# Optimization experiments

Hardware: AMD Instinct MI355X
Metric: run time of the kernel (lower is better)

## Reference

```python
import jax, jax.numpy as jnp
import numpy as np

N, E = 50000, 800000
IN, HID, HEADS = 512, 64, 2
NEG_SLOPE = 0.2

def _p(key, shape, fan_in):
    return jax.random.normal(key, shape, dtype=jnp.float32) * (1.0 / np.sqrt(fan_in))

def setup_inputs() -> dict:
    key = jax.random.key(0)
    ks = jax.random.split(key, 16)
    x = jax.random.normal(ks[0], (N, IN), dtype=jnp.float32)
    edge_index = jax.random.randint(ks[1], (2, E), 0, N)
    d = dict(x=x, edge_index=edge_index)
    # layer 0: in -> hidden*heads
    d['W0'] = _p(ks[2], (IN, HEADS * HID), IN)
    d['a_src0'] = _p(ks[3], (HEADS, HID), HID)
    d['a_dst0'] = _p(ks[4], (HEADS, HID), HID)
    d['b0'] = jnp.zeros((HEADS * HID,), jnp.float32)
    # layer 1: hidden*heads -> hidden*heads
    d['W1'] = _p(ks[5], (HEADS * HID, HEADS * HID), HEADS * HID)
    d['a_src1'] = _p(ks[6], (HEADS, HID), HID)
    d['a_dst1'] = _p(ks[7], (HEADS, HID), HID)
    d['b1'] = jnp.zeros((HEADS * HID,), jnp.float32)
    # layer 2: hidden*heads -> hidden, heads=1
    d['W2'] = _p(ks[8], (HEADS * HID, HID), HEADS * HID)
    d['a_src2'] = _p(ks[9], (1, HID), HID)
    d['a_dst2'] = _p(ks[10], (1, HID), HID)
    d['b2'] = jnp.zeros((HID,), jnp.float32)
    # MLP heads
    d['Wv'] = _p(ks[11], (HID, HID), HID)
    d['bv'] = jnp.zeros((HID,), jnp.float32)
    d['Wt'] = _p(ks[12], (HID, HID), HID)
    d['bt'] = jnp.zeros((HID,), jnp.float32)
    return d

def gat_conv(x, src, dst, W, a_src, a_dst, b, n_nodes):
    # PyG GATConv: linear -> per-node att scores -> edge leaky_relu -> segment softmax over dst -> weighted scatter-sum
    H, C = a_src.shape
    h = (x @ W).reshape(n_nodes, H, C)                     # [N,H,C]
    s = jnp.einsum('nhc,hc->nh', h, a_src)                 # [N,H]
    t = jnp.einsum('nhc,hc->nh', h, a_dst)                 # [N,H]
    e = jax.nn.leaky_relu(s[src] + t[dst], NEG_SLOPE)      # [Etot,H]
    m = jax.ops.segment_max(e, dst, num_segments=n_nodes)  # stable softmax per dst
    ex = jnp.exp(e - m[dst])
    den = jax.ops.segment_sum(ex, dst, num_segments=n_nodes)
    alpha = ex / (den[dst] + 1e-16)                        # [Etot,H]
    out = jax.ops.segment_sum(h[src] * alpha[..., None], dst, num_segments=n_nodes)
    return out.reshape(n_nodes, H * C) + b

def reference(x, edge_index, W0, a_src0, a_dst0, b0, W1, a_src1, a_dst1, b1,
              W2, a_src2, a_dst2, b2, Wv, bv, Wt, bt):
    n = x.shape[0]
    loop = jnp.arange(n)
    src = jnp.concatenate([edge_index[0], loop])  # add_self_loops=True
    dst = jnp.concatenate([edge_index[1], loop])
    h = gat_conv(x, src, dst, W0, a_src0, a_dst0, b0, n)
    h = jax.nn.relu(h)
    h = gat_conv(h, src, dst, W1, a_src1, a_dst1, b1, n)
    h = jax.nn.relu(h)
    h = gat_conv(h, src, dst, W2, a_src2, a_dst2, b2, n)  # heads=1 -> [N,HID]
    x_vision = jax.nn.relu(h @ Wv + bv)
    x_text = jax.nn.relu(h @ Wt + bt)
    return (h, x_vision, x_text)
```

## Files before the change

### kernel.cpp

```cpp
#include <hip/hip_runtime.h>
#include <hip/hip_bf16.h>
#include <hip/hip_fp16.h>
#include <math.h>

#define NN 50000
#define NE 800000

typedef unsigned short ushort_t;
typedef unsigned int uint_t;
typedef __attribute__((ext_vector_type(8))) short bf16x8;
typedef __attribute__((ext_vector_type(4))) float f32x4;

__device__ __forceinline__ float lrelu(float x) { return x >= 0.f ? x : 0.2f * x; }

__device__ __forceinline__ ushort_t f2bf_rn(float f) {
  uint_t u = __builtin_bit_cast(uint_t, f);
  uint_t r = u + 0x7FFFu + ((u >> 16) & 1u);
  return (ushort_t)(r >> 16);
}
__device__ __forceinline__ float bf2f(ushort_t h) {
  uint_t u = ((uint_t)h) << 16;
  return __builtin_bit_cast(float, u);
}

__global__ void count_kernel(const int* __restrict__ ei, int* __restrict__ counts, int E) {
  int e = blockIdx.x * blockDim.x + threadIdx.x;
  if (e < E) atomicAdd(&counts[ei[E + e]], 1);
}

__global__ __launch_bounds__(256) void scan_blocksum_kernel(const int* __restrict__ counts,
                                                            int* __restrict__ bsums, int n) {
  __shared__ int red[4];
  int i = blockIdx.x * 256 + threadIdx.x;
  int v = (i < n) ? counts[i] : 0;
#pragma unroll
  for (int off = 32; off > 0; off >>= 1) v += __shfl_down(v, off);
  if ((threadIdx.x & 63) == 0) red[threadIdx.x >> 6] = v;
  __syncthreads();
  if (threadIdx.x == 0) bsums[blockIdx.x] = red[0] + red[1] + red[2] + red[3];
}

__global__ __launch_bounds__(256) void scan_offsets_kernel(int* __restrict__ bsums, int nb) {
  __shared__ int sm[256];
  int tid = threadIdx.x;
  int v = (tid < nb) ? bsums[tid] : 0;
  sm[tid] = v;
  __syncthreads();
  for (int off = 1; off < 256; off <<= 1) {
    int u = (tid >= off) ? sm[tid - off] : 0;
    __syncthreads();
    sm[tid] += u;
    __syncthreads();
  }
  if (tid < nb) bsums[tid] = sm[tid] - v;
}

__global__ __launch_bounds__(256) void scan_final_kernel(const int* __restrict__ counts,
                                                         const int* __restrict__ boffs,
                                                         int* __restrict__ row_ptr, int n, int E) {
  __shared__ int sm[256];
  int tid = threadIdx.x;
  int i = blockIdx.x * 256 + tid;
  int v = (i < n) ? counts[i] : 0;
  int orig = v;
  sm[tid] = v;
  __syncthreads();
  for (int off = 1; off < 256; off <<= 1) {
    int u = (tid >= off) ? sm[tid - off] : 0;
    __syncthreads();
    sm[tid] += u;
    __syncthreads();
  }
  if (i < n) row_ptr[i] = boffs[blockIdx.x] + sm[tid] - orig;
  if (i == n) row_ptr[n] = E;
}

__global__ void fill_kernel(const int* __restrict__ ei, const int* __restrict__ row_ptr,
                            int* __restrict__ cursor, int* __restrict__ col_src, int E) {
  int e = blockIdx.x * blockDim.x + threadIdx.x;
  if (e < E) {
    int d = ei[E + e];
    int pos = row_ptr[d] + atomicAdd(&cursor[d], 1);
    col_src[pos] = ei[e];
  }
}

__global__ void prep_wt_kernel(const float* __restrict__ W, int Kdim, int C,
                               ushort_t* __restrict__ wth, ushort_t* __restrict__ wtl) {
  int t = blockIdx.x * blockDim.x + threadIdx.x;
  int nk = Kdim >> 4;
  if (t >= C * nk) return;
  int c = t / nk, kc = (t % nk) << 4;
  uint_t hw[8], lw[8];
#pragma unroll
  for (int i = 0; i < 8; ++i) {
    float f0 = W[(size_t)(kc + 2 * i) * C + c];
    float f1 = W[(size_t)(kc + 2 * i + 1) * C + c];
    ushort_t h0 = f2bf_rn(f0), h1 = f2bf_rn(f1);
    ushort_t l0 = f2bf_rn(f0 - bf2f(h0)), l1 = f2bf_rn(f1 - bf2f(h1));
    hw[i] = (uint_t)h0 | ((uint_t)h1 << 16);
    lw[i] = (uint_t)l0 | ((uint_t)l1 << 16);
  }
  uint_t* ph = (uint_t*)&wth[(size_t)c * Kdim + kc];
  uint_t* pl = (uint_t*)&wtl[(size_t)c * Kdim + kc];
  *(uint4*)ph = make_uint4(hw[0], hw[1], hw[2], hw[3]);
  *(uint4*)(ph + 4) = make_uint4(hw[4], hw[5], hw[6], hw[7]);
  *(uint4*)pl = make_uint4(lw[0], lw[1], lw[2], lw[3]);
  *(uint4*)(pl + 4) = make_uint4(lw[4], lw[5], lw[6], lw[7]);
}

template <int K>
__global__ __launch_bounds__(256, 2) void gemm_mfma_kernel(const float* __restrict__ A,
                                                           const ushort_t* __restrict__ wth,
                                                           const ushort_t* __restrict__ wtl,
                                                           float* __restrict__ out, int n) {
  __shared__ __align__(16) ushort_t ah[128][40];
  __shared__ __align__(16) ushort_t al[128][40];
  __shared__ __align__(16) ushort_t bh[128][40];
  __shared__ __align__(16) ushort_t bl[128][40];

  const int t = threadIdx.x;
  const int row0 = blockIdx.x * 128;
  const int srow = t >> 1;
  const int skq = (t & 1) * 16;

  const int lane = t & 63;
  const int wid = t >> 6;
  const int wm = wid >> 1, wn = wid & 1;
  const int r16 = lane & 15, g = lane >> 4;

  f32x4 acc[4][4];
#pragma unroll
  for (int i = 0; i < 4; ++i)
#pragma unroll
    for (int j = 0; j < 4; ++j) acc[i][j] = (f32x4)(0.f);

  for (int kt = 0; kt < K / 32; ++kt) {
    const int k0 = kt * 32;
    {
      uint_t hw[8], lw[8];
      if (row0 + srow < n) {
        const float* ap = &A[(size_t)(row0 + srow) * K + k0 + skq];
#pragma unroll
        for (int j = 0; j < 4; ++j) {
          float4 v = *(const float4*)(ap + j * 4);
          ushort_t h0 = f2bf_rn(v.x), h1 = f2bf_rn(v.y), h2 = f2bf_rn(v.z), h3 = f2bf_rn(v.w);
          ushort_t l0 = f2bf_rn(v.x - bf2f(h0)), l1 = f2bf_rn(v.y - bf2f(h1));
          ushort_t l2 = f2bf_rn(v.z - bf2f(h2)), l3 = f2bf_rn(v.w - bf2f(h3));
          hw[j * 2] = (uint_t)h0 | ((uint_t)h1 << 16);
          hw[j * 2 + 1] = (uint_t)h2 | ((uint_t)h3 << 16);
          lw[j * 2] = (uint_t)l0 | ((uint_t)l1 << 16);
          lw[j * 2 + 1] = (uint_t)l2 | ((uint_t)l3 << 16);
        }
      } else {
#pragma unroll
        for (int j = 0; j < 8; ++j) { hw[j] = 0; lw[j] = 0; }
      }
      *(uint4*)&ah[srow][skq] = make_uint4(hw[0], hw[1], hw[2], hw[3]);
      *(uint4*)&ah[srow][skq + 8] = make_uint4(hw[4], hw[5], hw[6], hw[7]);
      *(uint4*)&al[srow][skq] = make_uint4(lw[0], lw[1], lw[2], lw[3]);
      *(uint4*)&al[srow][skq + 8] = make_uint4(lw[4], lw[5], lw[6], lw[7]);
    }
    {
      const ushort_t* ph = &wth[(size_t)srow * K + k0 + skq];
      const ushort_t* pl = &wtl[(size_t)srow * K + k0 + skq];
      uint4 vh0 = *(const uint4*)ph;
      uint4 vh1 = *(const uint4*)(ph + 8);
      uint4 vl0 = *(const uint4*)pl;
      uint4 vl1 = *(const uint4*)(pl + 8);
      *(uint4*)&bh[srow][skq] = vh0;
      *(uint4*)&bh[srow][skq + 8] = vh1;
      *(uint4*)&bl[srow][skq] = vl0;
      *(uint4*)&bl[srow][skq + 8] = vl1;
    }
    __syncthreads();

    bf16x8 fah[4], fal[4], fbh[4], fbl[4];
#pragma unroll
    for (int mf = 0; mf < 4; ++mf) {
      fah[mf] = *(const bf16x8*)&ah[wm * 64 + mf * 16 + r16][g * 8];
      fal[mf] = *(const bf16x8*)&al[wm * 64 + mf * 16 + r16][g * 8];
    }
#pragma unroll
    for (int nf = 0; nf < 4; ++nf) {
      fbh[nf] = *(const bf16x8*)&bh[wn * 64 + nf * 16 + r16][g * 8];
      fbl[nf] = *(const bf16x8*)&bl[wn * 64 + nf * 16 + r16][g * 8];
    }
#pragma unroll
    for (int mf = 0; mf < 4; ++mf)
#pragma unroll
      for (int nf = 0; nf < 4; ++nf) {
        acc[mf][nf] = __builtin_amdgcn_mfma_f32_16x16x32_bf16(fah[mf], fbh[nf], acc[mf][nf], 0, 0, 0);
        acc[mf][nf] = __builtin_amdgcn_mfma_f32_16x16x32_bf16(fah[mf], fbl[nf], acc[mf][nf], 0, 0, 0);
        acc[mf][nf] = __builtin_amdgcn_mfma_f32_16x16x32_bf16(fal[mf], fbh[nf], acc[mf][nf], 0, 0, 0);
      }
    __syncthreads();
  }

#pragma unroll
  for (int mf = 0; mf < 4; ++mf) {
#pragma unroll
    for (int reg = 0; reg < 4; ++reg) {
      int row = row0 + wm * 64 + mf * 16 + g * 4 + reg;
      if (row < n) {
#pragma unroll
        for (int nf = 0; nf < 4; ++nf) {
          out[(size_t)row * 128 + wn * 64 + nf * 16 + r16] = acc[mf][nf][reg];
        }
      }
    }
  }
}

template <int K>
__global__ __launch_bounds__(256, 2) void gemm_mfma64_kernel(const float* __restrict__ A,
                                                             const ushort_t* __restrict__ wth,
                                                             const ushort_t* __restrict__ wtl,
                                                             const float* __restrict__ bias,
                                                             int do_relu,
                                                             float* __restrict__ out, int n) {
  __shared__ __align__(16) ushort_t ah[128][40];
  __shared__ __align__(16) ushort_t al[128][40];
  __shared__ __align__(16) ushort_t bh[64][40];
  __shared__ __align__(16) ushort_t bl[64][40];

  const int t = threadIdx.x;
  const int row0 = blockIdx.x * 128;
  const int srow = t >> 1;
  const int skq = (t & 1) * 16;
  const int bcol = t >> 2;
  const int bkq = (t & 3) * 8;

  const int lane = t & 63;
  const int wid = t >> 6;
  const int r16 = lane & 15, g = lane >> 4;

  f32x4 acc[2][4];
#pragma unroll
  for (int i = 0; i < 2; ++i)
#pragma unroll
    for (int j = 0; j < 4; ++j) acc[i][j] = (f32x4)(0.f);

  for (int kt = 0; kt < K / 32; ++kt) {
    const int k0 = kt * 32;
    {
      uint_t hw[8], lw[8];
      if (row0 + srow < n) {
        const float* ap = &A[(size_t)(row0 + srow) * K + k0 + skq];
#pragma unroll
        for (int j = 0; j < 4; ++j) {
          float4 v = *(const float4*)(ap + j * 4);
          ushort_t h0 = f2bf_rn(v.x), h1 = f2bf_rn(v.y), h2 = f2bf_rn(v.z), h3 = f2bf_rn(v.w);
          ushort_t l0 = f2bf_rn(v.x - bf2f(h0)), l1 = f2bf_rn(v.y - bf2f(h1));
          ushort_t l2 = f2bf_rn(v.z - bf2f(h2)), l3 = f2bf_rn(v.w - bf2f(h3));
          hw[j * 2] = (uint_t)h0 | ((uint_t)h1 << 16);
          hw[j * 2 + 1] = (uint_t)h2 | ((uint_t)h3 << 16);
          lw[j * 2] = (uint_t)l0 | ((uint_t)l1 << 16);
          lw[j * 2 + 1] = (uint_t)l2 | ((uint_t)l3 << 16);
        }
      } else {
#pragma unroll
        for (int j = 0; j < 8; ++j) { hw[j] = 0; lw[j] = 0; }
      }
      *(uint4*)&ah[srow][skq] = make_uint4(hw[0], hw[1], hw[2], hw[3]);
      *(uint4*)&ah[srow][skq + 8] = make_uint4(hw[4], hw[5], hw[6], hw[7]);
      *(uint4*)&al[srow][skq] = make_uint4(lw[0], lw[1], lw[2], lw[3]);
      *(uint4*)&al[srow][skq + 8] = make_uint4(lw[4], lw[5], lw[6], lw[7]);
    }
    {
      uint4 vh = *(const uint4*)&wth[(size_t)bcol * K + k0 + bkq];
      uint4 vl = *(const uint4*)&wtl[(size_t)bcol * K + k0 + bkq];
      *(uint4*)&bh[bcol][bkq] = vh;
      *(uint4*)&bl[bcol][bkq] = vl;
    }
    __syncthreads();

    bf16x8 fah[2], fal[2], fbh[4], fbl[4];
#pragma unroll
    for (int mf = 0; mf < 2; ++mf) {
      fah[mf] = *(const bf16x8*)&ah[wid * 32 + mf * 16 + r16][g * 8];
      fal[mf] = *(const bf16x8*)&al[wid * 32 + mf * 16 + r16][g * 8];
    }
#pragma unroll
    for (int nf = 0; nf < 4; ++nf) {
      fbh[nf] = *(const bf16x8*)&bh[nf * 16 + r16][g * 8];
      fbl[nf] = *(const bf16x8*)&bl[nf * 16 + r16][g * 8];
    }
#pragma unroll
    for (int mf = 0; mf < 2; ++mf)
#pragma unroll
      for (int nf = 0; nf < 4; ++nf) {
        acc[mf][nf] = __builtin_amdgcn_mfma_f32_16x16x32_bf16(fah[mf], fbh[nf], acc[mf][nf], 0, 0, 0);
        acc[mf][nf] = __builtin_amdgcn_mfma_f32_16x16x32_bf16(fah[mf], fbl[nf], acc[mf][nf], 0, 0, 0);
        acc[mf][nf] = __builtin_amdgcn_mfma_f32_16x16x32_bf16(fal[mf], fbh[nf], acc[mf][nf], 0, 0, 0);
      }
    __syncthreads();
  }

#pragma unroll
  for (int mf = 0; mf < 2; ++mf) {
#pragma unroll
    for (int reg = 0; reg < 4; ++reg) {
      int row = row0 + wid * 32 + mf * 16 + g * 4 + reg;
      if (row < n) {
#pragma unroll
        for (int nf = 0; nf < 4; ++nf) {
          int col = nf * 16 + r16;
          float v = acc[mf][nf][reg];
          if (bias) v += bias[col];
          if (do_relu) v = fmaxf(v, 0.f);
          out[(size_t)row * 64 + col] = v;
        }
      }
    }
  }
}

__global__ __launch_bounds__(256) void comb_att2_kernel(const float* __restrict__ P0,
                                                        const float* __restrict__ a_src,
                                                        const float* __restrict__ a_dst,
                                                        __half2* __restrict__ h2h,
                                                        float2* __restrict__ s2,
                                                        float2* __restrict__ t2, int n) {
  int wid = (blockIdx.x * 256 + threadIdx.x) >> 6;
  int lane = threadIdx.x & 63;
  if (wid >= n) return;
  float h0 = P0[(size_t)wid * 128 + lane];
  float h1 = P0[(size_t)wid * 128 + 64 + lane];
  h2h[(size_t)wid * 64 + lane] = __floats2half2_rn(h0, h1);
  float v0 = h0 * a_src[lane];
  float v1 = h1 * a_src[64 + lane];
  float v2 = h0 * a_dst[lane];
  float v3 = h1 * a_dst[64 + lane];
#pragma unroll
  for (int off = 32; off > 0; off >>= 1) {
    v0 += __shfl_xor(v0, off);
    v1 += __shfl_xor(v1, off);
    v2 += __shfl_xor(v2, off);
    v3 += __shfl_xor(v3, off);
  }
  if (lane == 0) {
    s2[wid] = make_float2(v0, v1);
    t2[wid] = make_float2(v2, v3);
  }
}

__global__ __launch_bounds__(256) void att1_kernel(const float* __restrict__ h,
                                                   const float* __restrict__ a_src,
                                                   const float* __restrict__ a_dst,
                                                   float* __restrict__ s, float* __restrict__ t,
                                                   __half* __restrict__ h16, int n) {
  int wid = (blockIdx.x * 256 + threadIdx.x) >> 6;
  int lane = threadIdx.x & 63;
  if (wid >= n) return;
  float h0 = h[(size_t)wid * 64 + lane];
  h16[(size_t)wid * 64 + lane] = __float2half(h0);
  float v0 = h0 * a_src[lane];
  float v1 = h0 * a_dst[lane];
#pragma unroll
  for (int off = 32; off > 0; off >>= 1) {
    v0 += __shfl_xor(v0, off);
    v1 += __shfl_xor(v1, off);
  }
  if (lane == 0) {
    s[wid] = v0;
    t[wid] = v1;
  }
}

__global__ __launch_bounds__(256) void agg2_kernel(const __half2* __restrict__ h2h,
                                                   const float2* __restrict__ s2,
                                                   const float2* __restrict__ t2,
                                                   const int* __restrict__ row_ptr,
                                                   const int* __restrict__ col_src,
                                                   const float* __restrict__ bias,
                                                   float* __restrict__ out, int n, int do_relu) {
  int wid = (blockIdx.x * 256 + threadIdx.x) >> 6;
  int lane = threadIdx.x & 63;
  if (wid >= n) return;
  const int node = wid;
  const float2 tt = t2[node];
  const float t0 = tt.x, t1 = tt.y;
  const int beg = row_ptr[node], end = row_ptr[node + 1];

  float2 sself = s2[node];
  const float e_self0 = lrelu(sself.x + t0);
  const float e_self1 = lrelu(sself.y + t1);

  const int i_own = beg + lane;
  int src_own = node;
  float e0_own = -1e30f, e1_own = -1e30f;
  if (i_own < end) {
    src_own = col_src[i_own];
    float2 sv = s2[src_own];
    e0_own = lrelu(sv.x + t0);
    e1_own = lrelu(sv.y + t1);
  }
  float m0 = fmaxf(e_self0, e0_own), m1 = fmaxf(e_self1, e1_own);
  for (int i = beg + 64 + lane; i < end; i += 64) {
    float2 sv = s2[col_src[i]];
    m0 = fmaxf(m0, lrelu(sv.x + t0));
    m1 = fmaxf(m1, lrelu(sv.y + t1));
  }
#pragma unroll
  for (int off = 32; off > 0; off >>= 1) {
    m0 = fmaxf(m0, __shfl_xor(m0, off));
    m1 = fmaxf(m1, __shfl_xor(m1, off));
  }

  float p0 = __expf(e_self0 - m0);
  float p1 = __expf(e_self1 - m1);
  float d0 = p0, d1 = p1;
  float2 hself = __half22float2(h2h[(size_t)node * 64 + lane]);
  float acc0 = p0 * hself.x;
  float acc1 = p1 * hself.y;

  for (int base = beg; base < end; base += 64) {
    int srcn;
    float q0, q1;
    if (base == beg) {
      srcn = src_own;
      q0 = (i_own < end) ? __expf(e0_own - m0) : 0.f;
      q1 = (i_own < end) ? __expf(e1_own - m1) : 0.f;
    } else {
      int i = base + lane;
      srcn = node;
      q0 = 0.f; q1 = 0.f;
      if (i < end) {
        srcn = col_src[i];
        float2 sv = s2[srcn];
        q0 = __expf(lrelu(sv.x + t0) - m0);
        q1 = __expf(lrelu(sv.y + t1) - m1);
      }
    }
    const int cnt = min(64, end - base);
    const int cnt4 = (cnt + 3) & ~3;
    int i0 = __shfl(srcn, 0), i1 = __shfl(srcn, 1), i2 = __shfl(srcn, 2), i3 = __shfl(srcn, 3);
    __half2 b0 = h2h[(size_t)i0 * 64 + lane];
    __half2 b1 = h2h[(size_t)i1 * 64 + lane];
    __half2 b2 = h2h[(size_t)i2 * 64 + lane];
    __half2 b3 = h2h[(size_t)i3 * 64 + lane];
    for (int j = 0; j < cnt4; j += 4) {
      float p00 = __shfl(q0, j),     p01 = __shfl(q1, j);
      float p10 = __shfl(q0, j + 1), p11 = __shfl(q1, j + 1);
      float p20 = __shfl(q0, j + 2), p21 = __shfl(q1, j + 2);
      float p30 = __shfl(q0, j + 3), p31 = __shfl(q1, j + 3);
      __half2 c0 = b0, c1 = b1, c2 = b2, c3 = b3;
      if (j + 4 < cnt4) {
        int n0 = __shfl(srcn, j + 4), n1 = __shfl(srcn, j + 5);
        int n2 = __shfl(srcn, j + 6), n3 = __shfl(srcn, j + 7);
        b0 = h2h[(size_t)n0 * 64 + lane];
        b1 = h2h[(size_t)n1 * 64 + lane];
        b2 = h2h[(size_t)n2 * 64 + lane];
        b3 = h2h[(size_t)n3 * 64 + lane];
      }
      float2 f0 = __half22float2(c0), f1 = __half22float2(c1);
      float2 f2 = __half22float2(c2), f3 = __half22float2(c3);
      d0 += p00 + p10 + p20 + p30;
      d1 += p01 + p11 + p21 + p31;
      acc0 = fmaf(p00, f0.x, acc0);
      acc1 = fmaf(p01, f0.y, acc1);
      acc0 = fmaf(p10, f1.x, acc0);
      acc1 = fmaf(p11, f1.y, acc1);
      acc0 = fmaf(p20, f2.x, acc0);
      acc1 = fmaf(p21, f2.y, acc1);
      acc0 = fmaf(p30, f3.x, acc0);
      acc1 = fmaf(p31, f3.y, acc1);
    }
  }

  float o0 = acc0 / (d0 + 1e-16f) + bias[lane];
  float o1 = acc1 / (d1 + 1e-16f) + bias[64 + lane];
  if (do_relu) {
    o0 = fmaxf(o0, 0.f);
    o1 = fmaxf(o1, 0.f);
  }
  out[(size_t)node * 128 + lane] = o0;
  out[(size_t)node * 128 + 64 + lane] = o1;
}

__global__ __launch_bounds__(256) void agg1_kernel(const __half* __restrict__ h16,
                                                   const float* __restrict__ s,
                                                   const float* __restrict__ t,
                                                   const int* __restrict__ row_ptr,
                                                   const int* __restrict__ col_src,
                                                   const float* __restrict__ bias,
                                                   float* __restrict__ out, int n) {
  int wid = (blockIdx.x * 256 + threadIdx.x) >> 6;
  int lane = threadIdx.x & 63;
  if (wid >= n) return;
  const int node = wid;
  const float t0 = t[node];
  const int beg = row_ptr[node], end = row_ptr[node + 1];

  const float e_self = lrelu(s[node] + t0);
  const int i_own = beg + lane;
  int src_own = node;
  float e_own = -1e30f;
  if (i_own < end) {
    src_own = col_src[i_own];
    e_own = lrelu(s[src_own] + t0);
  }
  float m0 = fmaxf(e_self, e_own);
  for (int i = beg + 64 + lane; i < end; i += 64) {
    m0 = fmaxf(m0, lrelu(s[col_src[i]] + t0));
  }
#pragma unroll
  for (int off = 32; off > 0; off >>= 1) m0 = fmaxf(m0, __shfl_xor(m0, off));

  float p = __expf(e_self - m0);
  float d0 = p;
  float acc0 = p * __half2float(h16[(size_t)node * 64 + lane]);

  for (int base = beg; base < end; base += 64) {
    int srcn;
    float q0;
    if (base == beg) {
      srcn = src_own;
      q0 = (i_own < end) ? __expf(e_own - m0) : 0.f;
    } else {
      int i = base + lane;
      srcn = node;
      q0 = 0.f;
      if (i < end) {
        srcn = col_src[i];
        q0 = __expf(lrelu(s[srcn] + t0) - m0);
      }
    }
    const int cnt = min(64, end - base);
    const int cnt4 = (cnt + 3) & ~3;
    int i0 = __shfl(srcn, 0), i1 = __shfl(srcn, 1), i2 = __shfl(srcn, 2), i3 = __shfl(srcn, 3);
    __half b0 = h16[(size_t)i0 * 64 + lane];
    __half b1 = h16[(size_t)i1 * 64 + lane];
    __half b2 = h16[(size_t)i2 * 64 + lane];
    __half b3 = h16[(size_t)i3 * 64 + lane];
    for (int j = 0; j < cnt4; j += 4) {
      float p0 = __shfl(q0, j),     p1 = __shfl(q0, j + 1);
      float p2 = __shfl(q0, j + 2), p3 = __shfl(q0, j + 3);
      float c0 = __half2float(b0), c1 = __half2float(b1);
      float c2 = __half2float(b2), c3 = __half2float(b3);
      if (j + 4 < cnt4) {
        int n0 = __shfl(srcn, j + 4), n1 = __shfl(srcn, j + 5);
        int n2 = __shfl(srcn, j + 6), n3 = __shfl(srcn, j + 7);
        b0 = h16[(size_t)n0 * 64 + lane];
        b1 = h16[(size_t)n1 * 64 + lane];
        b2 = h16[(size_t)n2 * 64 + lane];
        b3 = h16[(size_t)n3 * 64 + lane];
      }
      d0 += p0 + p1 + p2 + p3;
      acc0 = fmaf(p0, c0, acc0);
      acc0 = fmaf(p1, c1, acc0);
      acc0 = fmaf(p2, c2, acc0);
      acc0 = fmaf(p3, c3, acc0);
    }
  }
  out[(size_t)node * 64 + lane] = acc0 / (d0 + 1e-16f) + bias[lane];
}

extern "C" void kernel_launch(void* const* d_in, const int* in_sizes, int n_in,
                              void* d_out, int out_size, void* d_ws, size_t ws_size,
                              hipStream_t stream) {
  const float* x       = (const float*)d_in[0];
  const int*   ei      = (const int*)d_in[1];
  const float* W0      = (const float*)d_in[2];
  const float* a_src0  = (const float*)d_in[3];
  const float* a_dst0  = (const float*)d_in[4];
  const float* b0      = (const float*)d_in[5];
  const float* W1      = (const float*)d_in[6];
  const float* a_src1  = (const float*)d_in[7];
  const float* a_dst1  = (const float*)d_in[8];
  const float* b1      = (const float*)d_in[9];
  const float* W2      = (const float*)d_in[10];
  const float* a_src2  = (const float*)d_in[11];
  const float* a_dst2  = (const float*)d_in[12];
  const float* b2      = (const float*)d_in[13];
  const float* Wv      = (const float*)d_in[14];
  const float* bv      = (const float*)d_in[15];
  const float* Wt      = (const float*)d_in[16];
  const float* bt      = (const float*)d_in[17];

  const int n = NN, E = NE;
  const int NB = (n + 255) / 256;
  const int NBF = (n + 1 + 255) / 256;

  char* w = (char*)d_ws;
  int* counts  = (int*)w;   w += (size_t)n * 4;
  int* row_ptr = (int*)w;   w += (size_t)(n + 4) * 4;
  int* cursor  = (int*)w;   w += (size_t)n * 4;
  int* bsums   = (int*)w;   w += (size_t)256 * 4;
  int* col_src = (int*)w;   w += (size_t)E * 4;
  float2* s2   = (float2*)w; w += (size_t)n * 8;
  float2* t2   = (float2*)w; w += (size_t)n * 8;
  float* Abuf  = (float*)w;  w += (size_t)n * 128 * 4;
  float* P0    = (float*)w;  w += (size_t)n * 128 * 4;
  __half2* h2h = (__half2*)w; w += (size_t)n * 64 * 4;
  float* hbuf  = (float*)w;  w += (size_t)n * 64 * 4;
  __half* h16  = (__half*)w; w += (size_t)n * 64 * 2;
  ushort_t* wt0h = (ushort_t*)w; w += (size_t)128 * 512 * 2;
  ushort_t* wt0l = (ushort_t*)w; w += (size_t)128 * 512 * 2;
  ushort_t* wt1h = (ushort_t*)w; w += (size_t)128 * 128 * 2;
  ushort_t* wt1l = (ushort_t*)w; w += (size_t)128 * 128 * 2;
  ushort_t* wt2h = (ushort_t*)w; w += (size_t)64 * 128 * 2;
  ushort_t* wt2l = (ushort_t*)w; w += (size_t)64 * 128 * 2;
  ushort_t* wvh  = (ushort_t*)w; w += (size_t)64 * 64 * 2;
  ushort_t* wvl  = (ushort_t*)w; w += (size_t)64 * 64 * 2;
  ushort_t* wtth = (ushort_t*)w; w += (size_t)64 * 64 * 2;
  ushort_t* wttl = (ushort_t*)w; w += (size_t)64 * 64 * 2;

  float* s1 = (float*)s2;
  float* t1 = (float*)t2;

  float* out_h = (float*)d_out;
  float* out_v = out_h + (size_t)n * 64;
  float* out_t = out_v + (size_t)n * 64;

  hipMemsetAsync(counts, 0, (size_t)n * 4, stream);
  hipMemsetAsync(cursor, 0, (size_t)n * 4, stream);
  count_kernel<<<(E + 255) / 256, 256, 0, stream>>>(ei, counts, E);
  prep_wt_kernel<<<(128 * 32 + 255) / 256, 256, 0, stream>>>(W0, 512, 128, wt0h, wt0l);
  prep_wt_kernel<<<(128 * 8 + 255) / 256, 256, 0, stream>>>(W1, 128, 128, wt1h, wt1l);
  prep_wt_kernel<<<(64 * 8 + 255) / 256, 256, 0, stream>>>(W2, 128, 64, wt2h, wt2l);
  prep_wt_kernel<<<(64 * 4 + 255) / 256, 256, 0, stream>>>(Wv, 64, 64, wvh, wvl);
  prep_wt_kernel<<<(64 * 4 + 255) / 256, 256, 0, stream>>>(Wt, 64, 64, wtth, wttl);
  scan_blocksum_kernel<<<NB, 256, 0, stream>>>(counts, bsums, n);
  scan_offsets_kernel<<<1, 256, 0, stream>>>(bsums, NB);
  scan_final_kernel<<<NBF, 256, 0, stream>>>(counts, bsums, row_ptr, n, E);
  fill_kernel<<<(E + 255) / 256, 256, 0, stream>>>(ei, row_ptr, cursor, col_src, E);

  const int wgrid = (n + 3) / 4;
  const int g128 = (n + 127) / 128;

  gemm_mfma_kernel<512><<<g128, 256, 0, stream>>>(x, wt0h, wt0l, P0, n);
  comb_att2_kernel<<<wgrid, 256, 0, stream>>>(P0, a_src0, a_dst0, h2h, s2, t2, n);
  agg2_kernel<<<wgrid, 256, 0, stream>>>(h2h, s2, t2, row_ptr, col_src, b0, Abuf, n, 1);

  gemm_mfma_kernel<128><<<g128, 256, 0, stream>>>(Abuf, wt1h, wt1l, P0, n);
  comb_att2_kernel<<<wgrid, 256, 0, stream>>>(P0, a_src1, a_dst1, h2h, s2, t2, n);
  agg2_kernel<<<wgrid, 256, 0, stream>>>(h2h, s2, t2, row_ptr, col_src, b1, Abuf, n, 1);

  gemm_mfma64_kernel<128><<<g128, 256, 0, stream>>>(Abuf, wt2h, wt2l, nullptr, 0, hbuf, n);
  att1_kernel<<<wgrid, 256, 0, stream>>>(hbuf, a_src2, a_dst2, s1, t1, h16, n);
  agg1_kernel<<<wgrid, 256, 0, stream>>>(h16, s1, t1, row_ptr, col_src, b2, out_h, n);

  gemm_mfma64_kernel<64><<<g128, 256, 0, stream>>>(out_h, wvh, wvl, bv, 1, out_v, n);
  gemm_mfma64_kernel<64><<<g128, 256, 0, stream>>>(out_h, wtth, wttl, bt, 1, out_t, n);
}
```

Measured before the change: 358.0 us.

## Fuse attention scores into GEMM epilogues and merge setup and MLP-head launches

```diff
diff --git a/kernel.cpp b/kernel.cpp
--- a/kernel.cpp
+++ b/kernel.cpp
@@ -22,10 +22,59 @@
   uint_t u = ((uint_t)h) << 16;
   return __builtin_bit_cast(float, u);
 }
-
-__global__ void count_kernel(const int* __restrict__ ei, int* __restrict__ counts, int E) {
-  int e = blockIdx.x * blockDim.x + threadIdx.x;
-  if (e < E) atomicAdd(&counts[ei[E + e]], 1);
+__device__ __forceinline__ ushort_t f2h_bits(float f) {
+  __half h = __float2half(f);
+  return __builtin_bit_cast(ushort_t, h);
+}
+
+__device__ __forceinline__ void prep_dev(const float* __restrict__ W, int Kdim, int C,
+                                         ushort_t* __restrict__ wth, ushort_t* __restrict__ wtl,
+                                         int t) {
+  int nk = Kdim >> 4;
+  if (t >= C * nk) return;
+  int c = t / nk, kc = (t % nk) << 4;
+  uint_t hw[8], lw[8];
+#pragma unroll
+  for (int i = 0; i < 8; ++i) {
+    float f0 = W[(size_t)(kc + 2 * i) * C + c];
+    float f1 = W[(size_t)(kc + 2 * i + 1) * C + c];
+    ushort_t h0 = f2bf_rn(f0), h1 = f2bf_rn(f1);
+    ushort_t l0 = f2bf_rn(f0 - bf2f(h0)), l1 = f2bf_rn(f1 - bf2f(h1));
+    hw[i] = (uint_t)h0 | ((uint_t)h1 << 16);
+    lw[i] = (uint_t)l0 | ((uint_t)l1 << 16);
+  }
+  uint_t* ph = (uint_t*)&wth[(size_t)c * Kdim + kc];
+  uint_t* pl = (uint_t*)&wtl[(size_t)c * Kdim + kc];
+  *(uint4*)ph = make_uint4(hw[0], hw[1], hw[2], hw[3]);
+  *(uint4*)(ph + 4) = make_uint4(hw[4], hw[5], hw[6], hw[7]);
+  *(uint4*)pl = make_uint4(lw[0], lw[1], lw[2], lw[3]);
+  *(uint4*)(pl + 4) = make_uint4(lw[4], lw[5], lw[6], lw[7]);
+}
+
+#define CNT_BLOCKS 3125
+__global__ __launch_bounds__(256) void setup_kernel(const int* __restrict__ ei,
+                                                    int* __restrict__ counts,
+                                                    const float* __restrict__ W0, ushort_t* wt0h, ushort_t* wt0l,
+                                                    const float* __restrict__ W1, ushort_t* wt1h, ushort_t* wt1l,
+                                                    const float* __restrict__ W2, ushort_t* wt2h, ushort_t* wt2l,
+                                                    const float* __restrict__ Wv, const float* __restrict__ Wt,
+                                                    ushort_t* wHh, ushort_t* wHl) {
+  int b = blockIdx.x;
+  if (b < CNT_BLOCKS) {
+    int e = b * 256 + threadIdx.x;
+    if (e < NE) atomicAdd(&counts[ei[NE + e]], 1);
+    return;
+  }
+  b -= CNT_BLOCKS;
+  if (b < 16) { prep_dev(W0, 512, 128, wt0h, wt0l, b * 256 + threadIdx.x); return; }
+  b -= 16;
+  if (b < 4) { prep_dev(W1, 128, 128, wt1h, wt1l, b * 256 + threadIdx.x); return; }
+  b -= 4;
+  if (b < 2) { prep_dev(W2, 128, 64, wt2h, wt2l, b * 256 + threadIdx.x); return; }
+  b -= 2;
+  if (b < 1) { prep_dev(Wv, 64, 64, wHh, wHl, b * 256 + threadIdx.x); return; }
+  b -= 1;
+  prep_dev(Wt, 64, 64, wHh + 64 * 64, wHl + 64 * 64, b * 256 + threadIdx.x);
 }
 
 __global__ __launch_bounds__(256) void scan_blocksum_kernel(const int* __restrict__ counts,
@@ -57,7 +106,8 @@
 
 __global__ __launch_bounds__(256) void scan_final_kernel(const int* __restrict__ counts,
                                                          const int* __restrict__ boffs,
-                                                         int* __restrict__ row_ptr, int n, int E) {
+                                                         int* __restrict__ row_ptr,
+                                                         int* __restrict__ cursor, int n, int E) {
   __shared__ int sm[256];
   int tid = threadIdx.x;
   int i = blockIdx.x * 256 + tid;
@@ -71,7 +121,10 @@
     sm[tid] += u;
     __syncthreads();
   }
-  if (i < n) row_ptr[i] = boffs[blockIdx.x] + sm[tid] - orig;
+  if (i < n) {
+    row_ptr[i] = boffs[blockIdx.x] + sm[tid] - orig;
+    cursor[i] = 0;
+  }
   if (i == n) row_ptr[n] = E;
 }
 
@@ -85,39 +138,20 @@
   }
 }
 
-__global__ void prep_wt_kernel(const float* __restrict__ W, int Kdim, int C,
-                               ushort_t* __restrict__ wth, ushort_t* __restrict__ wtl) {
-  int t = blockIdx.x * blockDim.x + threadIdx.x;
-  int nk = Kdim >> 4;
-  if (t >= C * nk) return;
-  int c = t / nk, kc = (t % nk) << 4;
-  uint_t hw[8], lw[8];
-#pragma unroll
-  for (int i = 0; i < 8; ++i) {
-    float f0 = W[(size_t)(kc + 2 * i) * C + c];
-    float f1 = W[(size_t)(kc + 2 * i + 1) * C + c];
-    ushort_t h0 = f2bf_rn(f0), h1 = f2bf_rn(f1);
-    ushort_t l0 = f2bf_rn(f0 - bf2f(h0)), l1 = f2bf_rn(f1 - bf2f(h1));
-    hw[i] = (uint_t)h0 | ((uint_t)h1 << 16);
-    lw[i] = (uint_t)l0 | ((uint_t)l1 << 16);
-  }
-  uint_t* ph = (uint_t*)&wth[(size_t)c * Kdim + kc];
-  uint_t* pl = (uint_t*)&wtl[(size_t)c * Kdim + kc];
-  *(uint4*)ph = make_uint4(hw[0], hw[1], hw[2], hw[3]);
-  *(uint4*)(ph + 4) = make_uint4(hw[4], hw[5], hw[6], hw[7]);
-  *(uint4*)pl = make_uint4(lw[0], lw[1], lw[2], lw[3]);
-  *(uint4*)(pl + 4) = make_uint4(lw[4], lw[5], lw[6], lw[7]);
-}
-
 template <int K>
-__global__ __launch_bounds__(256, 2) void gemm_mfma_kernel(const float* __restrict__ A,
-                                                           const ushort_t* __restrict__ wth,
-                                                           const ushort_t* __restrict__ wtl,
-                                                           float* __restrict__ out, int n) {
-  __shared__ __align__(16) ushort_t ah[128][40];
-  __shared__ __align__(16) ushort_t al[128][40];
-  __shared__ __align__(16) ushort_t bh[128][40];
-  __shared__ __align__(16) ushort_t bl[128][40];
+__global__ __launch_bounds__(256, 2) void gemm_mfma_att_kernel(const float* __restrict__ A,
+                                                               const ushort_t* __restrict__ wth,
+                                                               const ushort_t* __restrict__ wtl,
+                                                               const float* __restrict__ a_src,
+                                                               const float* __restrict__ a_dst,
+                                                               __half2* __restrict__ h2h,
+                                                               float* __restrict__ s_arr,
+                                                               float* __restrict__ t_arr, int n) {
+  __shared__ __align__(16) ushort_t smem[20480];
+  ushort_t (*ah)[40] = (ushort_t(*)[40])smem;
+  ushort_t (*al)[40] = (ushort_t(*)[40])(smem + 5120);
+  ushort_t (*bh)[40] = (ushort_t(*)[40])(smem + 10240);
+  ushort_t (*bl)[40] = (ushort_t(*)[40])(smem + 15360);
 
   const int t = threadIdx.x;
   const int row0 = blockIdx.x * 128;
@@ -197,32 +231,73 @@
     __syncthreads();
   }
 
+  const int head = wn;
+  float asv[4], adv[4];
+#pragma unroll
+  for (int nf = 0; nf < 4; ++nf) {
+    asv[nf] = a_src[head * 64 + nf * 16 + r16];
+    adv[nf] = a_dst[head * 64 + nf * 16 + r16];
+  }
 #pragma unroll
   for (int mf = 0; mf < 4; ++mf) {
 #pragma unroll
     for (int reg = 0; reg < 4; ++reg) {
+      float sp = 0.f, tp = 0.f;
+#pragma unroll
+      for (int nf = 0; nf < 4; ++nf) {
+        sp = fmaf(acc[mf][nf][reg], asv[nf], sp);
+        tp = fmaf(acc[mf][nf][reg], adv[nf], tp);
+      }
+#pragma unroll
+      for (int off = 1; off < 16; off <<= 1) {
+        sp += __shfl_xor(sp, off);
+        tp += __shfl_xor(tp, off);
+      }
       int row = row0 + wm * 64 + mf * 16 + g * 4 + reg;
-      if (row < n) {
-#pragma unroll
-        for (int nf = 0; nf < 4; ++nf) {
-          out[(size_t)row * 128 + wn * 64 + nf * 16 + r16] = acc[mf][nf][reg];
-        }
-      }
+      if (r16 == 0 && row < n) {
+        s_arr[row * 2 + head] = sp;
+        t_arr[row * 2 + head] = tp;
+      }
+    }
+  }
+
+  ushort_t* hstage = smem;
+#pragma unroll
+  for (int mf = 0; mf < 4; ++mf)
+#pragma unroll
+    for (int nf = 0; nf < 4; ++nf)
+#pragma unroll
+      for (int reg = 0; reg < 4; ++reg) {
+        int rl = wm * 64 + mf * 16 + g * 4 + reg;
+        int col = (nf * 16 + r16) * 2 + head;
+        hstage[rl * 136 + col] = f2h_bits(acc[mf][nf][reg]);
+      }
+  __syncthreads();
+#pragma unroll
+  for (int it = 0; it < 8; ++it) {
+    int idx = t + it * 256;
+    int r = idx >> 4, ch = idx & 15;
+    if (row0 + r < n) {
+      *(uint4*)((char*)h2h + (size_t)(row0 + r) * 256 + ch * 16) =
+          *(const uint4*)&hstage[r * 136 + ch * 8];
     }
   }
 }
 
 template <int K>
-__global__ __launch_bounds__(256, 2) void gemm_mfma64_kernel(const float* __restrict__ A,
-                                                             const ushort_t* __restrict__ wth,
-                                                             const ushort_t* __restrict__ wtl,
-                                                             const float* __restrict__ bias,
-                                                             int do_relu,
-                                                             float* __restrict__ out, int n) {
-  __shared__ __align__(16) ushort_t ah[128][40];
-  __shared__ __align__(16) ushort_t al[128][40];
-  __shared__ __align__(16) ushort_t bh[64][40];
-  __shared__ __align__(16) ushort_t bl[64][40];
+__global__ __launch_bounds__(256, 2) void gemm_mfma64_att_kernel(const float* __restrict__ A,
+                                                                 const ushort_t* __restrict__ wth,
+                                                                 const ushort_t* __restrict__ wtl,
+                                                                 const float* __restrict__ a_src,
+                                                                 const float* __restrict__ a_dst,
+                                                                 __half* __restrict__ h16,
+                                                                 float* __restrict__ s1,
+                                                                 float* __restrict__ t1, int n) {
+  __shared__ __align__(16) ushort_t smem[15360];
+  ushort_t (*ah)[40] = (ushort_t(*)[40])smem;
+  ushort_t (*al)[40] = (ushort_t(*)[40])(smem + 5120);
+  ushort_t (*bh)[40] = (ushort_t(*)[40])(smem + 10240);
+  ushort_t (*bl)[40] = (ushort_t(*)[40])(smem + 12800);
 
   const int t = threadIdx.x;
   const int row0 = blockIdx.x * 128;
@@ -297,74 +372,166 @@
     __syncthreads();
   }
 
+  float asv[4], adv[4];
+#pragma unroll
+  for (int nf = 0; nf < 4; ++nf) {
+    asv[nf] = a_src[nf * 16 + r16];
+    adv[nf] = a_dst[nf * 16 + r16];
+  }
 #pragma unroll
   for (int mf = 0; mf < 2; ++mf) {
 #pragma unroll
     for (int reg = 0; reg < 4; ++reg) {
+      float sp = 0.f, tp = 0.f;
+#pragma unroll
+      for (int nf = 0; nf < 4; ++nf) {
+        sp = fmaf(acc[mf][nf][reg], asv[nf], sp);
+        tp = fmaf(acc[mf][nf][reg], adv[nf], tp);
+      }
+#pragma unroll
+      for (int off = 1; off < 16; off <<= 1) {
+        sp += __shfl_xor(sp, off);
+        tp += __shfl_xor(tp, off);
+      }
       int row = row0 + wid * 32 + mf * 16 + g * 4 + reg;
+      if (r16 == 0 && row < n) {
+        s1[row] = sp;
+        t1[row] = tp;
+      }
+    }
+  }
+
+  ushort_t* hstage = smem;
+#pragma unroll
+  for (int mf = 0; mf < 2; ++mf)
+#pragma unroll
+    for (int nf = 0; nf < 4; ++nf)
+#pragma unroll
+      for (int reg = 0; reg < 4; ++reg) {
+        int rl = wid * 32 + mf * 16 + g * 4 + reg;
+        int col = nf * 16 + r16;
+        hstage[rl * 72 + col] = f2h_bits(acc[mf][nf][reg]);
+      }
+  __syncthreads();
+#pragma unroll
+  for (int it = 0; it < 4; ++it) {
+    int idx = t + it * 256;
+    int r = idx >> 3, ch = idx & 7;
+    if (row0 + r < n) {
+      *(uint4*)((char*)h16 + (size_t)(row0 + r) * 128 + ch * 16) =
+          *(const uint4*)&hstage[r * 72 + ch * 8];
+    }
+  }
+}
+
+__global__ __launch_bounds__(256, 2) void gemm_heads_kernel(const float* __restrict__ A,
+                                                            const ushort_t* __restrict__ wth,
+                                                            const ushort_t* __restrict__ wtl,
+                                                            const float* __restrict__ bv,
+                                                            const float* __restrict__ bt,
+                                                            float* __restrict__ out_v,
+                                                            float* __restrict__ out_t, int n) {
+  constexpr int K = 64;
+  __shared__ __align__(16) ushort_t smem[20480];
+  ushort_t (*ah)[40] = (ushort_t(*)[40])smem;
+  ushort_t (*al)[40] = (ushort_t(*)[40])(smem + 5120);
+  ushort_t (*bh)[40] = (ushort_t(*)[40])(smem + 10240);
+  ushort_t (*bl)[40] = (ushort_t(*)[40])(smem + 15360);
+
+  const int t = threadIdx.x;
+  const int row0 = blockIdx.x * 128;
+  const int srow = t >> 1;
+  const int skq = (t & 1) * 16;
+
+  const int lane = t & 63;
+  const int wid = t >> 6;
+  const int wm = wid >> 1, wn = wid & 1;
+  const int r16 = lane & 15, g = lane >> 4;
+
+  f32x4 acc[4][4];
+#pragma unroll
+  for (int i = 0; i < 4; ++i)
+#pragma unroll
+    for (int j = 0; j < 4; ++j) acc[i][j] = (f32x4)(0.f);
+
+  for (int kt = 0; kt < K / 32; ++kt) {
+    const int k0 = kt * 32;
+    {
+      uint_t hw[8], lw[8];
+      if (row0 + srow < n) {
+        const float* ap = &A[(size_t)(row0 + srow) * K + k0 + skq];
+#pragma unroll
+        for (int j = 0; j < 4; ++j) {
+          float4 v = *(const float4*)(ap + j * 4);
+          ushort_t h0 = f2bf_rn(v.x), h1 = f2bf_rn(v.y), h2 = f2bf_rn(v.z), h3 = f2bf_rn(v.w);
+          ushort_t l0 = f2bf_rn(v.x - bf2f(h0)), l1 = f2bf_rn(v.y - bf2f(h1));
+          ushort_t l2 = f2bf_rn(v.z - bf2f(h2)), l3 = f2bf_rn(v.w - bf2f(h3));
+          hw[j * 2] = (uint_t)h0 | ((uint_t)h1 << 16);
+          hw[j * 2 + 1] = (uint_t)h2 | ((uint_t)h3 << 16);
+          lw[j * 2] = (uint_t)l0 | ((uint_t)l1 << 16);
+          lw[j * 2 + 1] = (uint_t)l2 | ((uint_t)l3 << 16);
+        }
+      } else {
+#pragma unroll
+        for (int j = 0; j < 8; ++j) { hw[j] = 0; lw[j] = 0; }
+      }
+      *(uint4*)&ah[srow][skq] = make_uint4(hw[0], hw[1], hw[2], hw[3]);
+      *(uint4*)&ah[srow][skq + 8] = make_uint4(hw[4], hw[5], hw[6], hw[7]);
+      *(uint4*)&al[srow][skq] = make_uint4(lw[0], lw[1], lw[2], lw[3]);
+      *(uint4*)&al[srow][skq + 8] = make_uint4(lw[4], lw[5], lw[6], lw[7]);
+    }
+    {
+      const ushort_t* ph = &wth[(size_t)srow * K + k0 + skq];
+      const ushort_t* pl = &wtl[(size_t)srow * K + k0 + skq];
+      uint4 vh0 = *(const uint4*)ph;
+      uint4 vh1 = *(const uint4*)(ph + 8);
+      uint4 vl0 = *(const uint4*)pl;
+      uint4 vl1 = *(const uint4*)(pl + 8);
+      *(uint4*)&bh[srow][skq] = vh0;
+      *(uint4*)&bh[srow][skq + 8] = vh1;
+      *(uint4*)&bl[srow][skq] = vl0;
+      *(uint4*)&bl[srow][skq + 8] = vl1;
+    }
+    __syncthreads();
+
+    bf16x8 fah[4], fal[4], fbh[4], fbl[4];
+#pragma unroll
+    for (int mf = 0; mf < 4; ++mf) {
+      fah[mf] = *(const bf16x8*)&ah[wm * 64 + mf * 16 + r16][g * 8];
+      fal[mf] = *(const bf16x8*)&al[wm * 64 + mf * 16 + r16][g * 8];
+    }
+#pragma unroll
+    for (int nf = 0; nf < 4; ++nf) {
+      fbh[nf] = *(const bf16x8*)&bh[wn * 64 + nf * 16 + r16][g * 8];
+      fbl[nf] = *(const bf16x8*)&bl[wn * 64 + nf * 16 + r16][g * 8];
+    }
+#pragma unroll
+    for (int mf = 0; mf < 4; ++mf)
+#pragma unroll
+      for (int nf = 0; nf < 4; ++nf) {
+        acc[mf][nf] = __builtin_amdgcn_mfma_f32_16x16x32_bf16(fah[mf], fbh[nf], acc[mf][nf], 0, 0, 0);
+        acc[mf][nf] = __builtin_amdgcn_mfma_f32_16x16x32_bf16(fah[mf], fbl[nf], acc[mf][nf], 0, 0, 0);
+        acc[mf][nf] = __builtin_amdgcn_mfma_f32_16x16x32_bf16(fal[mf], fbh[nf], acc[mf][nf], 0, 0, 0);
+      }
+    __syncthreads();
+  }
+
+  const float* bias = wn ? bt : bv;
+  float* outp = wn ? out_t : out_v;
+#pragma unroll
+  for (int mf = 0; mf < 4; ++mf) {
+#pragma unroll
+    for (int reg = 0; reg < 4; ++reg) {
+      int row = row0 + wm * 64 + mf * 16 + g * 4 + reg;
       if (row < n) {
 #pragma unroll
         for (int nf = 0; nf < 4; ++nf) {
-          int col = nf * 16 + r16;
-          float v = acc[mf][nf][reg];
-          if (bias) v += bias[col];
-          if (do_relu) v = fmaxf(v, 0.f);
-          out[(size_t)row * 64 + col] = v;
+          int c = nf * 16 + r16;
+          float v = fmaxf(acc[mf][nf][reg] + bias[c], 0.f);
+          outp[(size_t)row * 64 + c] = v;
         }
       }
     }
-  }
-}
-
-__global__ __launch_bounds__(256) void comb_att2_kernel(const float* __restrict__ P0,
-                                                        const float* __restrict__ a_src,
-                                                        const float* __restrict__ a_dst,
-                                                        __half2* __restrict__ h2h,
-                                                        float2* __restrict__ s2,
-                                                        float2* __restrict__ t2, int n) {
-  int wid = (blockIdx.x * 256 + threadIdx.x) >> 6;
-  int lane = threadIdx.x & 63;
-  if (wid >= n) return;
-  float h0 = P0[(size_t)wid * 128 + lane];
-  float h1 = P0[(size_t)wid * 128 + 64 + lane];
-  h2h[(size_t)wid * 64 + lane] = __floats2half2_rn(h0, h1);
-  float v0 = h0 * a_src[lane];
-  float v1 = h1 * a_src[64 + lane];
-  float v2 = h0 * a_dst[lane];
-  float v3 = h1 * a_dst[64 + lane];
-#pragma unroll
-  for (int off = 32; off > 0; off >>= 1) {
-    v0 += __shfl_xor(v0, off);
-    v1 += __shfl_xor(v1, off);
-    v2 += __shfl_xor(v2, off);
-    v3 += __shfl_xor(v3, off);
-  }
-  if (lane == 0) {
-    s2[wid] = make_float2(v0, v1);
-    t2[wid] = make_float2(v2, v3);
-  }
-}
-
-__global__ __launch_bounds__(256) void att1_kernel(const float* __restrict__ h,
-                                                   const float* __restrict__ a_src,
-                                                   const float* __restrict__ a_dst,
-                                                   float* __restrict__ s, float* __restrict__ t,
-                                                   __half* __restrict__ h16, int n) {
-  int wid = (blockIdx.x * 256 + threadIdx.x) >> 6;
-  int lane = threadIdx.x & 63;
-  if (wid >= n) return;
-  float h0 = h[(size_t)wid * 64 + lane];
-  h16[(size_t)wid * 64 + lane] = __float2half(h0);
-  float v0 = h0 * a_src[lane];
-  float v1 = h0 * a_dst[lane];
-#pragma unroll
-  for (int off = 32; off > 0; off >>= 1) {
-    v0 += __shfl_xor(v0, off);
-    v1 += __shfl_xor(v1, off);
-  }
-  if (lane == 0) {
-    s[wid] = v0;
-    t[wid] = v1;
   }
 }
 
@@ -589,12 +756,10 @@
   int* cursor  = (int*)w;   w += (size_t)n * 4;
   int* bsums   = (int*)w;   w += (size_t)256 * 4;
   int* col_src = (int*)w;   w += (size_t)E * 4;
-  float2* s2   = (float2*)w; w += (size_t)n * 8;
-  float2* t2   = (float2*)w; w += (size_t)n * 8;
+  float* s_arr = (float*)w; w += (size_t)n * 2 * 4;
+  float* t_arr = (float*)w; w += (size_t)n * 2 * 4;
   float* Abuf  = (float*)w;  w += (size_t)n * 128 * 4;
-  float* P0    = (float*)w;  w += (size_t)n * 128 * 4;
   __half2* h2h = (__half2*)w; w += (size_t)n * 64 * 4;
-  float* hbuf  = (float*)w;  w += (size_t)n * 64 * 4;
   __half* h16  = (__half*)w; w += (size_t)n * 64 * 2;
   ushort_t* wt0h = (ushort_t*)w; w += (size_t)128 * 512 * 2;
   ushort_t* wt0l = (ushort_t*)w; w += (size_t)128 * 512 * 2;
@@ -602,46 +767,40 @@
   ushort_t* wt1l = (ushort_t*)w; w += (size_t)128 * 128 * 2;
   ushort_t* wt2h = (ushort_t*)w; w += (size_t)64 * 128 * 2;
   ushort_t* wt2l = (ushort_t*)w; w += (size_t)64 * 128 * 2;
-  ushort_t* wvh  = (ushort_t*)w; w += (size_t)64 * 64 * 2;
-  ushort_t* wvl  = (ushort_t*)w; w += (size_t)64 * 64 * 2;
-  ushort_t* wtth = (ushort_t*)w; w += (size_t)64 * 64 * 2;
-  ushort_t* wttl = (ushort_t*)w; w += (size_t)64 * 64 * 2;
-
-  float* s1 = (float*)s2;
-  float* t1 = (float*)t2;
+  ushort_t* wHh  = (ushort_t*)w; w += (size_t)128 * 64 * 2;
+  ushort_t* wHl  = (ushort_t*)w; w += (size_t)128 * 64 * 2;
+
+  float* s1 = s_arr;
+  float* t1 = t_arr;
 
   float* out_h = (float*)d_out;
   float* out_v = out_h + (size_t)n * 64;
   float* out_t = out_v + (size_t)n * 64;
 
   hipMemsetAsync(counts, 0, (size_t)n * 4, stream);
-  hipMemsetAsync(cursor, 0, (size_t)n * 4, stream);
-  count_kernel<<<(E + 255) / 256, 256, 0, stream>>>(ei, counts, E);
-  prep_wt_kernel<<<(128 * 32 + 255) / 256, 256, 0, stream>>>(W0, 512, 128, wt0h, wt0l);
-  prep_wt_kernel<<<(128 * 8 + 255) / 256, 256, 0, stream>>>(W1, 128, 128, wt1h, wt1l);
-  prep_wt_kernel<<<(64 * 8 + 255) / 256, 256, 0, stream>>>(W2, 128, 64, wt2h, wt2l);
-  prep_wt_kernel<<<(64 * 4 + 255) / 256, 256, 0, stream>>>(Wv, 64, 64, wvh, wvl);
-  prep_wt_kernel<<<(64 * 4 + 255) / 256, 256, 0, stream>>>(Wt, 64, 64, wtth, wttl);
+  setup_kernel<<<CNT_BLOCKS + 16 + 4 + 2 + 1 + 1, 256, 0, stream>>>(
+      ei, counts, W0, wt0h, wt0l, W1, wt1h, wt1l, W2, wt2h, wt2l, Wv, Wt, wHh, wHl);
   scan_blocksum_kernel<<<NB, 256, 0, stream>>>(counts, bsums, n);
   scan_offsets_kernel<<<1, 256, 0, stream>>>(bsums, NB);
-  scan_final_kernel<<<NBF, 256, 0, stream>>>(counts, bsums, row_ptr, n, E);
+  scan_final_kernel<<<NBF, 256, 0, stream>>>(counts, bsums, row_ptr, cursor, n, E);
   fill_kernel<<<(E + 255) / 256, 256, 0, stream>>>(ei, row_ptr, cursor, col_src, E);
 
   const int wgrid = (n + 3) / 4;
   const int g128 = (n + 127) / 128;
 
-  gemm_mfma_kernel<512><<<g128, 256, 0, stream>>>(x, wt0h, wt0l, P0, n);
-  comb_att2_kernel<<<wgrid, 256, 0, stream>>>(P0, a_src0, a_dst0, h2h, s2, t2, n);
-  agg2_kernel<<<wgrid, 256, 0, stream>>>(h2h, s2, t2, row_ptr, col_src, b0, Abuf, n, 1);
-
-  gemm_mfma_kernel<128><<<g128, 256, 0, stream>>>(Abuf, wt1h, wt1l, P0, n);
-  comb_att2_kernel<<<wgrid, 256, 0, stream>>>(P0, a_src1, a_dst1, h2h, s2, t2, n);
-  agg2_kernel<<<wgrid, 256, 0, stream>>>(h2h, s2, t2, row_ptr, col_src, b1, Abuf, n, 1);
-
-  gemm_mfma64_kernel<128><<<g128, 256, 0, stream>>>(Abuf, wt2h, wt2l, nullptr, 0, hbuf, n);
-  att1_kernel<<<wgrid, 256, 0, stream>>>(hbuf, a_src2, a_dst2, s1, t1, h16, n);
+  gemm_mfma_att_kernel<512><<<g128, 256, 0, stream>>>(x, wt0h, wt0l, a_src0, a_dst0,
+                                                      h2h, s_arr, t_arr, n);
+  agg2_kernel<<<wgrid, 256, 0, stream>>>(h2h, (const float2*)s_arr, (const float2*)t_arr,
+                                         row_ptr, col_src, b0, Abuf, n, 1);
+
+  gemm_mfma_att_kernel<128><<<g128, 256, 0, stream>>>(Abuf, wt1h, wt1l, a_src1, a_dst1,
+                                                      h2h, s_arr, t_arr, n);
+  agg2_kernel<<<wgrid, 256, 0, stream>>>(h2h, (const float2*)s_arr, (const float2*)t_arr,
+                                         row_ptr, col_src, b1, Abuf, n, 1);
+
+  gemm_mfma64_att_kernel<128><<<g128, 256, 0, stream>>>(Abuf, wt2h, wt2l, a_src2, a_dst2,
+                                                        h16, s1, t1, n);
   agg1_kernel<<<wgrid, 256, 0, stream>>>(h16, s1, t1, row_ptr, col_src, b2, out_h, n);
 
-  gemm_mfma64_kernel<64><<<g128, 256, 0, stream>>>(out_h, wvh, wvl, bv, 1, out_v, n);
-  gemm_mfma64_kernel<64><<<g128, 256, 0, stream>>>(out_h, wtth, wttl, bt, 1, out_t, n);
-}
+  gemm_heads_kernel<<<g128, 256, 0, stream>>>(out_h, wHh, wHl, bv, bt, out_v, out_t, n);
+}
```

Result: faster. 301.7 us (-15.7%).
